# Kernel optimization log

Hardware: AMD Instinct MI355X
Metric: run time of the kernel (lower is better)

## Reference

```python
import jax, jax.numpy as jnp
import numpy as np

NUM_LAYERS = 3

def setup_inputs() -> dict:
    key = jax.random.key(0)
    ks = jax.random.split(key, 9)
    B, T, ND, H, LD, L = 128, 512, 128, 512, 128, NUM_LAYERS
    s = 0.05
    return {
        "noise_seq": jax.random.normal(ks[0], (B, T, ND), jnp.float32),
        "h_coupled": jax.random.normal(ks[1], (L, B, H), jnp.float32),
        "Wx0": jax.random.normal(ks[2], (ND, 4 * H), jnp.float32) * s,
        "Wxr": jax.random.normal(ks[3], (L - 1, H, 4 * H), jnp.float32) * s,
        "Wh": jax.random.normal(ks[4], (L, H, 4 * H), jnp.float32) * s,
        "Wc": jax.random.normal(ks[5], (L, H, 4 * H), jnp.float32) * s,
        "b": jnp.zeros((L, 4 * H), jnp.float32),
        "Wout": jax.random.normal(ks[6], (H, LD), jnp.float32) * s,
        "bout": jnp.zeros((LD,), jnp.float32),
    }

def _cell(x, h, c, h_cpl, Wx, Wh_i, Wc_i, b_i):
    # gates: [B, 4H] = x@Wx + h@Wh + h_cpl@Wc + b
    gates = x @ Wx + h @ Wh_i + h_cpl @ Wc_i + b_i
    i_g, f_g, g_g, o_g = jnp.split(gates, 4, axis=-1)
    c_new = jax.nn.sigmoid(f_g) * c + jax.nn.sigmoid(i_g) * jnp.tanh(g_g)
    h_new = jax.nn.sigmoid(o_g) * jnp.tanh(c_new)
    return h_new, c_new

def reference(noise_seq, h_coupled, Wx0, Wxr, Wh, Wc, b, Wout, bout):
    B, T, _ = noise_seq.shape
    L, _, H = h_coupled.shape

    def step(carry, x_t):
        h, c = carry  # each [L, B, H]
        hs, cs = [], []
        inp = x_t
        for i in range(L):
            Wx = Wx0 if i == 0 else Wxr[i - 1]
            h_new, c_new = _cell(inp, h[i], c[i], h_coupled[i], Wx, Wh[i], Wc[i], b[i])
            hs.append(h_new)
            cs.append(c_new)
            inp = h_new
        out_t = jax.nn.sigmoid(inp @ Wout + bout)  # [B, latent]
        return (jnp.stack(hs), jnp.stack(cs)), out_t

    h0 = jnp.zeros((L, B, H), noise_seq.dtype)
    c0 = jnp.zeros((L, B, H), noise_seq.dtype)
    xs = jnp.swapaxes(noise_seq, 0, 1)  # [T, B, ND]
    (h_fin, _), outs = jax.lax.scan(step, (h0, c0), xs)
    return jnp.swapaxes(outs, 0, 1), h_fin  # [B, T, latent], [L, B, H]
```

## Files before the change

kernel.cpp:

```cpp
#include <hip/hip_runtime.h>
#include <hip/hip_bf16.h>


typedef unsigned short ushort_t;

using frag_ab = __attribute__((ext_vector_type(8))) short;
using frag_cd = __attribute__((ext_vector_type(4))) float;

#define B_   128
#define T_   512
#define ND_  128
#define H_   512
#define G_   2048
#define LD_  128

#define OFF_WHH   0u
#define OFF_WHL   3145728u
#define OFF_WXH   6291456u
#define OFF_WXL   8650752u
#define OFF_WCH   11010048u
#define OFF_WCL   14155776u
#define OFF_WOUT  17301504u
#define OFF_HCH   17367040u
#define OFF_HCL   17563648u
#define OFF_HBH   17760256u
#define OFF_HBL   18153472u
#define OFF_SCR   18546688u
#define USH_BYTES 37224448u
#define FOFF_C     0u
#define FOFF_CTERM 196608u

__device__ inline float sig_(float x)  { return 1.0f / (1.0f + __expf(-x)); }
__device__ inline float tanh_(float x) { return 2.0f / (1.0f + __expf(-2.0f * x)) - 1.0f; }

__device__ inline ushort_t f2b(float f) {
    __hip_bfloat16 h = __float2bfloat16(f);
    return __builtin_bit_cast(unsigned short, h);
}
__device__ inline float b2f(ushort_t u) {
    unsigned int v = ((unsigned int)u) << 16;
    return __builtin_bit_cast(float, v);
}

__global__ void swz_kernel(const float* __restrict__ src,
                           ushort_t* __restrict__ dhi, ushort_t* __restrict__ dlo,
                           int K, int N) {
    int tid = blockIdx.x * 256 + threadIdx.x;
    int total = (K >> 5) * (N >> 4) * 64;
    if (tid >= total) return;
    int lane = tid & 63;
    int rest = tid >> 6;
    int NF = N >> 4;
    int nf = rest % NF;
    int kb = rest / NF;
    int kbase = kb * 32 + (lane >> 4) * 8;
    int n = nf * 16 + (lane & 15);
    union { ushort_t u[8]; uint4 v; } thi, tlo;
#pragma unroll
    for (int j = 0; j < 8; ++j) {
        float v = src[(size_t)(kbase + j) * N + n];
        ushort_t hi = f2b(v);
        thi.u[j] = hi;
        tlo.u[j] = f2b(v - b2f(hi));
    }
    *(uint4*)(dhi + (size_t)tid * 8) = thi.v;
    *(uint4*)(dlo + (size_t)tid * 8) = tlo.v;
}

__global__ void cvt_kernel(const float* __restrict__ src,
                           ushort_t* __restrict__ dhi, ushort_t* __restrict__ dlo, int n) {
    int i = blockIdx.x * 256 + threadIdx.x;
    if (i >= n) return;
    float v = src[i];
    ushort_t hi = f2b(v);
    dhi[i] = hi;
    dlo[i] = f2b(v - b2f(hi));
}

__device__ inline void mfma_seg3(const ushort_t* __restrict__ Ah,
                                 const ushort_t* __restrict__ Al,
                                 const ushort_t* __restrict__ Bh,
                                 const ushort_t* __restrict__ Bl,
                                 int rowA, int cg, int nkb, frag_cd acc[4]) {
    int lane = threadIdx.x & 63;
    int koff = (lane >> 4) * 8;
#pragma unroll 2
    for (int kb = 0; kb < nkb; ++kb) {
        frag_ab ah = *(const frag_ab*)(Ah + (size_t)rowA * H_ + kb * 32 + koff);
        frag_ab al = *(const frag_ab*)(Al + (size_t)rowA * H_ + kb * 32 + koff);
#pragma unroll
        for (int q = 0; q < 4; ++q) {
            size_t bo = ((size_t)(kb * 128 + q * 32 + cg) * 64 + lane) * 8;
            frag_ab bh = *(const frag_ab*)(Bh + bo);
            frag_ab bl = *(const frag_ab*)(Bl + bo);
            acc[q] = __builtin_amdgcn_mfma_f32_16x16x32_bf16(ah, bh, acc[q], 0, 0, 0);
            acc[q] = __builtin_amdgcn_mfma_f32_16x16x32_bf16(ah, bl, acc[q], 0, 0, 0);
            acc[q] = __builtin_amdgcn_mfma_f32_16x16x32_bf16(al, bh, acc[q], 0, 0, 0);
        }
    }
}

__global__ __launch_bounds__(256) void cterm_kernel(char* __restrict__ ws,
                                                    const float* __restrict__ bias) {
    ushort_t* wsU = (ushort_t*)ws;
    float* wsF = (float*)(ws + USH_BYTES);
    int lane = threadIdx.x & 63, w = threadIdx.x >> 6;
    int bid = blockIdx.x;
    int layer = bid >> 6;
    int sub = bid & 63;
    int rg = sub >> 5, cg = sub & 31;
    int m = lane & 15, kq = lane >> 4;
    int r0 = rg * 64 + w * 16;
    int rowA = r0 + m;
    frag_cd acc[4] = {};
    mfma_seg3(wsU + OFF_HCH + layer * 65536, wsU + OFF_HCL + layer * 65536,
              wsU + OFF_WCH + (size_t)layer * 1048576, wsU + OFF_WCL + (size_t)layer * 1048576,
              rowA, cg, 16, acc);
    float* ct = wsF + FOFF_CTERM + (size_t)layer * 262144;
#pragma unroll
    for (int reg = 0; reg < 4; ++reg) {
        int row = r0 + kq * 4 + reg;
#pragma unroll
        for (int q = 0; q < 4; ++q) {
            int gcol = q * 512 + cg * 16 + m;
            ct[(size_t)row * G_ + gcol] = acc[q][reg] + bias[layer * G_ + gcol];
        }
    }
}

__device__ inline void seg_accum64k(const ushort_t* __restrict__ Ah,
                                    const ushort_t* __restrict__ Al,
                                    const ushort_t* __restrict__ Bh,
                                    const ushort_t* __restrict__ Bl,
                                    int r0, int cg, int kb0, int nkb, frag_cd acc[4][4]) {
    int lane = threadIdx.x & 63;
    int m = lane & 15;
    int koff = (lane >> 4) * 8;
#pragma unroll 2
    for (int kb = kb0; kb < kb0 + nkb; ++kb) {
        frag_ab ah[4], al[4];
#pragma unroll
        for (int rt = 0; rt < 4; ++rt) {
            size_t ao = (size_t)(r0 + rt * 16 + m) * H_ + kb * 32 + koff;
            ah[rt] = *(const frag_ab*)(Ah + ao);
            al[rt] = *(const frag_ab*)(Al + ao);
        }
#pragma unroll
        for (int q = 0; q < 4; ++q) {
            size_t bo = ((size_t)(kb * 128 + q * 32 + cg) * 64 + lane) * 8;
            frag_ab bh = *(const frag_ab*)(Bh + bo);
            frag_ab bl = *(const frag_ab*)(Bl + bo);
#pragma unroll
            for (int rt = 0; rt < 4; ++rt) {
                acc[rt][q] = __builtin_amdgcn_mfma_f32_16x16x32_bf16(ah[rt], bh, acc[rt][q], 0, 0, 0);
                acc[rt][q] = __builtin_amdgcn_mfma_f32_16x16x32_bf16(ah[rt], bl, acc[rt][q], 0, 0, 0);
                acc[rt][q] = __builtin_amdgcn_mfma_f32_16x16x32_bf16(al[rt], bh, acc[rt][q], 0, 0, 0);
            }
        }
    }
}

__global__ __launch_bounds__(256) void tick_kernel(const float* __restrict__ noise,
                                                   char* __restrict__ ws,
                                                   float* __restrict__ out,
                                                   const float* __restrict__ bout,
                                                   int tick) {
    __shared__ float ex[4][4096];

    ushort_t* wsU = (ushort_t*)ws;
    float* wsF = (float*)(ws + USH_BYTES);
    int lane = threadIdx.x & 63;
    int w = threadIdx.x >> 6;
    int bid = blockIdx.x;
    int m = lane & 15, kq = lane >> 4;
    int koff = kq * 8;

    if (bid < 192) {
        int rg64 = bid / 96;
        int u = bid % 96;
        int layer = u >> 5;
        int cg = u & 31;
        int s = tick - layer;
        if (s < 0 || s >= T_) return;
        int r0 = rg64 * 64;
        frag_cd acc[4][4] = {};

        if (layer == 0) {
            const ushort_t* Bh = wsU + OFF_WXH;
            const ushort_t* Bl = wsU + OFF_WXL;
            int kb = w;
            frag_ab ah[4], al[4];
#pragma unroll
            for (int rt = 0; rt < 4; ++rt) {
                const float* np = noise +
                    ((size_t)(r0 + rt * 16 + m) * T_ + s) * ND_ + kb * 32 + koff;
                float4 f0 = *(const float4*)np;
                float4 f1 = *(const float4*)(np + 4);
                float xf[8] = {f0.x, f0.y, f0.z, f0.w, f1.x, f1.y, f1.z, f1.w};
#pragma unroll
                for (int j = 0; j < 8; ++j) {
                    ushort_t hi = f2b(xf[j]);
                    ah[rt][j] = (short)hi;
                    al[rt][j] = (short)f2b(xf[j] - b2f(hi));
                }
            }
#pragma unroll
            for (int q = 0; q < 4; ++q) {
                size_t bo = ((size_t)(kb * 128 + q * 32 + cg) * 64 + lane) * 8;
                frag_ab bh = *(const frag_ab*)(Bh + bo);
                frag_ab bl = *(const frag_ab*)(Bl + bo);
#pragma unroll
                for (int rt = 0; rt < 4; ++rt) {
                    acc[rt][q] = __builtin_amdgcn_mfma_f32_16x16x32_bf16(ah[rt], bh, acc[rt][q], 0, 0, 0);
                    acc[rt][q] = __builtin_amdgcn_mfma_f32_16x16x32_bf16(ah[rt], bl, acc[rt][q], 0, 0, 0);
                    acc[rt][q] = __builtin_amdgcn_mfma_f32_16x16x32_bf16(al[rt], bh, acc[rt][q], 0, 0, 0);
                }
            }
        } else {
            unsigned hb = (unsigned)((layer - 1) * 2 + (s & 1)) * 65536u;
            seg_accum64k(wsU + OFF_HBH + hb, wsU + OFF_HBL + hb,
                         wsU + OFF_WXH + 262144u + (size_t)(layer - 1) * 1048576,
                         wsU + OFF_WXL + 262144u + (size_t)(layer - 1) * 1048576,
                         r0, cg, w * 4, 4, acc);
        }
        if (s > 0) {
            unsigned hb = (unsigned)(layer * 2 + ((s - 1) & 1)) * 65536u;
            seg_accum64k(wsU + OFF_HBH + hb, wsU + OFF_HBL + hb,
                         wsU + OFF_WHH + (size_t)layer * 1048576,
                         wsU + OFF_WHL + (size_t)layer * 1048576,
                         r0, cg, w * 4, 4, acc);
        }

        {
            float* eb = &ex[w][0];
#pragma unroll
            for (int rt = 0; rt < 4; ++rt)
#pragma unroll
                for (int q = 0; q < 4; ++q)
#pragma unroll
                    for (int reg = 0; reg < 4; ++reg)
                        eb[(rt * 16 + kq * 4 + reg) * 64 + q * 16 + m] = acc[rt][q][reg];
        }
        __syncthreads();

        const float* ct = wsF + FOFF_CTERM + (size_t)layer * 262144;
        float* cst = wsF + FOFF_C + layer * 65536;
        ushort_t* hhi = wsU + OFF_HBH + (layer * 2 + (s & 1)) * 65536;
        ushort_t* hlo = wsU + OFF_HBL + (layer * 2 + (s & 1)) * 65536;
        int tid = threadIdx.x;
#pragma unroll
        for (int ee = 0; ee < 4; ++ee) {
            int e = tid + ee * 256;
            int row = e >> 4;
            int hcol = e & 15;
            int grow = r0 + row;
            int hc = cg * 16 + hcol;
            int rb = row * 64 + hcol;
            float gi = ex[0][rb +  0] + ex[1][rb +  0] + ex[2][rb +  0] + ex[3][rb +  0];
            float gf = ex[0][rb + 16] + ex[1][rb + 16] + ex[2][rb + 16] + ex[3][rb + 16];
            float gg = ex[0][rb + 32] + ex[1][rb + 32] + ex[2][rb + 32] + ex[3][rb + 32];
            float go = ex[0][rb + 48] + ex[1][rb + 48] + ex[2][rb + 48] + ex[3][rb + 48];
            const float* cr = ct + (size_t)grow * G_ + hc;
            gi += cr[0]; gf += cr[512]; gg += cr[1024]; go += cr[1536];
            float cp = (s > 0) ? cst[grow * H_ + hc] : 0.0f;
            float cn = sig_(gf) * cp + sig_(gi) * tanh_(gg);
            float hn = sig_(go) * tanh_(cn);
            cst[grow * H_ + hc] = cn;
            ushort_t hi = f2b(hn);
            hhi[grow * H_ + hc] = hi;
            hlo[grow * H_ + hc] = f2b(hn - b2f(hi));
            if (s == T_ - 1)
                out[8388608u + (size_t)layer * 65536 + grow * H_ + hc] = hn;
        }
    } else {
        int sp = tick - 3;
        if (sp < 0 || sp >= T_) return;
        int owid = (bid - 192) * 4 + w;
        int rg = owid >> 1;
        int ch = owid & 1;
        int r0o = rg * 32;
        const ushort_t* A  = wsU + OFF_HBH + (4 + (sp & 1)) * 65536;
        const ushort_t* Bw = wsU + OFF_WOUT;
        frag_cd acc[2][4] = {};
#pragma unroll 2
        for (int kb = 0; kb < 16; ++kb) {
            frag_ab a[2];
#pragma unroll
            for (int rt = 0; rt < 2; ++rt)
                a[rt] = *(const frag_ab*)(A + (size_t)(r0o + rt * 16 + m) * H_ + kb * 32 + koff);
#pragma unroll
            for (int cf = 0; cf < 4; ++cf) {
                frag_ab b = *(const frag_ab*)(Bw + ((size_t)(kb * 8 + ch * 4 + cf) * 64 + lane) * 8);
#pragma unroll
                for (int rt = 0; rt < 2; ++rt)
                    acc[rt][cf] = __builtin_amdgcn_mfma_f32_16x16x32_bf16(a[rt], b, acc[rt][cf], 0, 0, 0);
            }
        }
#pragma unroll
        for (int rt = 0; rt < 2; ++rt)
#pragma unroll
            for (int cf = 0; cf < 4; ++cf)
#pragma unroll
                for (int reg = 0; reg < 4; ++reg) {
                    int row = r0o + rt * 16 + kq * 4 + reg;
                    int oc = ch * 64 + cf * 16 + m;
                    out[((size_t)row * T_ + sp) * LD_ + oc] =
                        sig_(acc[rt][cf][reg] + bout[oc]);
                }
    }
}

extern "C" void kernel_launch(void* const* d_in, const int* in_sizes, int n_in,
                              void* d_out, int out_size, void* d_ws, size_t ws_size,
                              hipStream_t stream) {
    const float* noise = (const float*)d_in[0];
    const float* hcpl  = (const float*)d_in[1];
    const float* Wx0   = (const float*)d_in[2];
    const float* Wxr   = (const float*)d_in[3];
    const float* Wh    = (const float*)d_in[4];
    const float* Wc    = (const float*)d_in[5];
    const float* bias  = (const float*)d_in[6];
    const float* Wout  = (const float*)d_in[7];
    const float* bout  = (const float*)d_in[8];
    float* out = (float*)d_out;
    char* ws = (char*)d_ws;
    ushort_t* wsU = (ushort_t*)ws;

    auto launch_swz = [&](const float* src, unsigned ohi, unsigned olo, int K, int N) {
        int total = (K / 32) * (N / 16) * 64;
        swz_kernel<<<(total + 255) / 256, 256, 0, stream>>>(src, wsU + ohi, wsU + olo, K, N);
    };
    for (int l = 0; l < 3; ++l)
        launch_swz(Wh + (size_t)l * H_ * G_, OFF_WHH + l * 1048576u, OFF_WHL + l * 1048576u, H_, G_);
    launch_swz(Wx0, OFF_WXH, OFF_WXL, ND_, G_);
    for (int l = 0; l < 2; ++l)
        launch_swz(Wxr + (size_t)l * H_ * G_, OFF_WXH + 262144u + l * 1048576u,
                   OFF_WXL + 262144u + l * 1048576u, H_, G_);
    for (int l = 0; l < 3; ++l)
        launch_swz(Wc + (size_t)l * H_ * G_, OFF_WCH + l * 1048576u, OFF_WCL + l * 1048576u, H_, G_);
    launch_swz(Wout, OFF_WOUT, OFF_SCR, H_, LD_);
    cvt_kernel<<<(3 * B_ * H_ + 255) / 256, 256, 0, stream>>>(hcpl, wsU + OFF_HCH, wsU + OFF_HCL,
                                                              3 * B_ * H_);
    cterm_kernel<<<192, 256, 0, stream>>>(ws, bias);

    for (int t = 0; t < 515; ++t)
        tick_kernel<<<194, 256, 0, stream>>>(noise, ws, out, bout, t);
}
```

Before: 8.513 ms.

## Replace per-tick launches with persistent kernel using per-step flag dataflow

The 515 per-tick kernel launches are replaced by one persistent kernel of 194 blocks. Each block loops over time steps and waits on per-layer, per-step atomic counters in workspace instead of relying on kernel boundaries. Hidden-state buffers grow from double to quadruple buffering so layers can run up to several steps apart, and the cell state moves from global memory into registers. This removes launch overhead and the global barrier on every tick. In exchange it depends on all 194 blocks being resident at the same time, and adds spin-wait and fence costs.

```diff
diff --git a/kernel.cpp b/kernel.cpp
--- a/kernel.cpp
+++ b/kernel.cpp
@@ -24,11 +24,14 @@
 #define OFF_HCH   17367040u
 #define OFF_HCL   17563648u
 #define OFF_HBH   17760256u
-#define OFF_HBL   18153472u
-#define OFF_SCR   18546688u
-#define USH_BYTES 37224448u
+#define OFF_HBL   18546688u
+#define OFF_SCR   19333120u
+#define USH_BYTES 38797312u
 #define FOFF_C     0u
 #define FOFF_CTERM 196608u
+#define FOFF_FLAGS 983040u
+
+#define FIDX(l2, s) ((((l2) * 512) + (s)) * 16)
 
 __device__ inline float sig_(float x)  { return 1.0f / (1.0f + __expf(-x)); }
 __device__ inline float tanh_(float x) { return 2.0f / (1.0f + __expf(-2.0f * x)) - 1.0f; }
@@ -40,6 +43,11 @@
 __device__ inline float b2f(ushort_t u) {
     unsigned int v = ((unsigned int)u) << 16;
     return __builtin_bit_cast(float, v);
+}
+
+__device__ inline void spin_ge(int* p, int tgt) {
+    while (__hip_atomic_load(p, __ATOMIC_RELAXED, __HIP_MEMORY_SCOPE_AGENT) < tgt)
+        __builtin_amdgcn_s_sleep(1);
 }
 
 __global__ void swz_kernel(const float* __restrict__ src,
@@ -75,6 +83,12 @@
     ushort_t hi = f2b(v);
     dhi[i] = hi;
     dlo[i] = f2b(v - b2f(hi));
+}
+
+__global__ void zero_flags_kernel(char* __restrict__ ws) {
+    int* flg = (int*)(ws + USH_BYTES) + FOFF_FLAGS;
+    int i = blockIdx.x * 256 + threadIdx.x;
+    if (i < 8 * 512 * 16) flg[i] = 0;
 }
 
 __device__ inline void mfma_seg3(const ushort_t* __restrict__ Ah,
@@ -160,15 +174,15 @@
     }
 }
 
-__global__ __launch_bounds__(256) void tick_kernel(const float* __restrict__ noise,
-                                                   char* __restrict__ ws,
-                                                   float* __restrict__ out,
-                                                   const float* __restrict__ bout,
-                                                   int tick) {
+__global__ __launch_bounds__(256) void persist_kernel(const float* __restrict__ noise,
+                                                      char* __restrict__ ws,
+                                                      float* __restrict__ out,
+                                                      const float* __restrict__ bout) {
     __shared__ float ex[4][4096];
 
     ushort_t* wsU = (ushort_t*)ws;
     float* wsF = (float*)(ws + USH_BYTES);
+    int* flg = (int*)wsF + FOFF_FLAGS;
     int lane = threadIdx.x & 63;
     int w = threadIdx.x >> 6;
     int bid = blockIdx.x;
@@ -180,133 +194,160 @@
         int u = bid % 96;
         int layer = u >> 5;
         int cg = u & 31;
-        int s = tick - layer;
-        if (s < 0 || s >= T_) return;
         int r0 = rg64 * 64;
-        frag_cd acc[4][4] = {};
-
-        if (layer == 0) {
-            const ushort_t* Bh = wsU + OFF_WXH;
-            const ushort_t* Bl = wsU + OFF_WXL;
-            int kb = w;
-            frag_ab ah[4], al[4];
-#pragma unroll
-            for (int rt = 0; rt < 4; ++rt) {
-                const float* np = noise +
-                    ((size_t)(r0 + rt * 16 + m) * T_ + s) * ND_ + kb * 32 + koff;
-                float4 f0 = *(const float4*)np;
-                float4 f1 = *(const float4*)(np + 4);
-                float xf[8] = {f0.x, f0.y, f0.z, f0.w, f1.x, f1.y, f1.z, f1.w};
-#pragma unroll
-                for (int j = 0; j < 8; ++j) {
-                    ushort_t hi = f2b(xf[j]);
-                    ah[rt][j] = (short)hi;
-                    al[rt][j] = (short)f2b(xf[j] - b2f(hi));
-                }
-            }
-#pragma unroll
-            for (int q = 0; q < 4; ++q) {
-                size_t bo = ((size_t)(kb * 128 + q * 32 + cg) * 64 + lane) * 8;
-                frag_ab bh = *(const frag_ab*)(Bh + bo);
-                frag_ab bl = *(const frag_ab*)(Bl + bo);
+        int l2 = layer * 2 + rg64;
+        const float* ct = wsF + FOFF_CTERM + (size_t)layer * 262144;
+        float creg[4] = {0.0f, 0.0f, 0.0f, 0.0f};
+
+        for (int s = 0; s < T_; ++s) {
+            if (threadIdx.x == 0) {
+                if (layer > 0) spin_ge(&flg[FIDX(l2 - 2, s)], 32);
+                if (s > 0)     spin_ge(&flg[FIDX(l2, s - 1)], 32);
+                if (s >= 4) {
+                    if (layer < 2) spin_ge(&flg[FIDX(l2 + 2, s - 4)], 32);
+                    else           spin_ge(&flg[FIDX(6 + rg64, s - 4)], 1);
+                }
+                __builtin_amdgcn_fence(__ATOMIC_ACQUIRE, "agent");
+            }
+            __syncthreads();
+
+            frag_cd acc[4][4] = {};
+            if (layer == 0) {
+                const ushort_t* Bh = wsU + OFF_WXH;
+                const ushort_t* Bl = wsU + OFF_WXL;
+                int kb = w;
+                frag_ab ah[4], al[4];
 #pragma unroll
                 for (int rt = 0; rt < 4; ++rt) {
-                    acc[rt][q] = __builtin_amdgcn_mfma_f32_16x16x32_bf16(ah[rt], bh, acc[rt][q], 0, 0, 0);
-                    acc[rt][q] = __builtin_amdgcn_mfma_f32_16x16x32_bf16(ah[rt], bl, acc[rt][q], 0, 0, 0);
-                    acc[rt][q] = __builtin_amdgcn_mfma_f32_16x16x32_bf16(al[rt], bh, acc[rt][q], 0, 0, 0);
-                }
-            }
-        } else {
-            unsigned hb = (unsigned)((layer - 1) * 2 + (s & 1)) * 65536u;
-            seg_accum64k(wsU + OFF_HBH + hb, wsU + OFF_HBL + hb,
-                         wsU + OFF_WXH + 262144u + (size_t)(layer - 1) * 1048576,
-                         wsU + OFF_WXL + 262144u + (size_t)(layer - 1) * 1048576,
-                         r0, cg, w * 4, 4, acc);
-        }
-        if (s > 0) {
-            unsigned hb = (unsigned)(layer * 2 + ((s - 1) & 1)) * 65536u;
-            seg_accum64k(wsU + OFF_HBH + hb, wsU + OFF_HBL + hb,
-                         wsU + OFF_WHH + (size_t)layer * 1048576,
-                         wsU + OFF_WHL + (size_t)layer * 1048576,
-                         r0, cg, w * 4, 4, acc);
-        }
-
-        {
-            float* eb = &ex[w][0];
-#pragma unroll
-            for (int rt = 0; rt < 4; ++rt)
-#pragma unroll
-                for (int q = 0; q < 4; ++q)
-#pragma unroll
-                    for (int reg = 0; reg < 4; ++reg)
-                        eb[(rt * 16 + kq * 4 + reg) * 64 + q * 16 + m] = acc[rt][q][reg];
-        }
-        __syncthreads();
-
-        const float* ct = wsF + FOFF_CTERM + (size_t)layer * 262144;
-        float* cst = wsF + FOFF_C + layer * 65536;
-        ushort_t* hhi = wsU + OFF_HBH + (layer * 2 + (s & 1)) * 65536;
-        ushort_t* hlo = wsU + OFF_HBL + (layer * 2 + (s & 1)) * 65536;
-        int tid = threadIdx.x;
-#pragma unroll
-        for (int ee = 0; ee < 4; ++ee) {
-            int e = tid + ee * 256;
-            int row = e >> 4;
-            int hcol = e & 15;
-            int grow = r0 + row;
-            int hc = cg * 16 + hcol;
-            int rb = row * 64 + hcol;
-            float gi = ex[0][rb +  0] + ex[1][rb +  0] + ex[2][rb +  0] + ex[3][rb +  0];
-            float gf = ex[0][rb + 16] + ex[1][rb + 16] + ex[2][rb + 16] + ex[3][rb + 16];
-            float gg = ex[0][rb + 32] + ex[1][rb + 32] + ex[2][rb + 32] + ex[3][rb + 32];
-            float go = ex[0][rb + 48] + ex[1][rb + 48] + ex[2][rb + 48] + ex[3][rb + 48];
-            const float* cr = ct + (size_t)grow * G_ + hc;
-            gi += cr[0]; gf += cr[512]; gg += cr[1024]; go += cr[1536];
-            float cp = (s > 0) ? cst[grow * H_ + hc] : 0.0f;
-            float cn = sig_(gf) * cp + sig_(gi) * tanh_(gg);
-            float hn = sig_(go) * tanh_(cn);
-            cst[grow * H_ + hc] = cn;
-            ushort_t hi = f2b(hn);
-            hhi[grow * H_ + hc] = hi;
-            hlo[grow * H_ + hc] = f2b(hn - b2f(hi));
-            if (s == T_ - 1)
-                out[8388608u + (size_t)layer * 65536 + grow * H_ + hc] = hn;
+                    const float* np = noise +
+                        ((size_t)(r0 + rt * 16 + m) * T_ + s) * ND_ + kb * 32 + koff;
+                    float4 f0 = *(const float4*)np;
+                    float4 f1 = *(const float4*)(np + 4);
+                    float xf[8] = {f0.x, f0.y, f0.z, f0.w, f1.x, f1.y, f1.z, f1.w};
+#pragma unroll
+                    for (int j = 0; j < 8; ++j) {
+                        ushort_t hi = f2b(xf[j]);
+                        ah[rt][j] = (short)hi;
+                        al[rt][j] = (short)f2b(xf[j] - b2f(hi));
+                    }
+                }
+#pragma unroll
+                for (int q = 0; q < 4; ++q) {
+                    size_t bo = ((size_t)(kb * 128 + q * 32 + cg) * 64 + lane) * 8;
+                    frag_ab bh = *(const frag_ab*)(Bh + bo);
+                    frag_ab bl = *(const frag_ab*)(Bl + bo);
+#pragma unroll
+                    for (int rt = 0; rt < 4; ++rt) {
+                        acc[rt][q] = __builtin_amdgcn_mfma_f32_16x16x32_bf16(ah[rt], bh, acc[rt][q], 0, 0, 0);
+                        acc[rt][q] = __builtin_amdgcn_mfma_f32_16x16x32_bf16(ah[rt], bl, acc[rt][q], 0, 0, 0);
+                        acc[rt][q] = __builtin_amdgcn_mfma_f32_16x16x32_bf16(al[rt], bh, acc[rt][q], 0, 0, 0);
+                    }
+                }
+            } else {
+                unsigned hb = (unsigned)((layer - 1) * 4 + (s & 3)) * 65536u;
+                seg_accum64k(wsU + OFF_HBH + hb, wsU + OFF_HBL + hb,
+                             wsU + OFF_WXH + 262144u + (size_t)(layer - 1) * 1048576,
+                             wsU + OFF_WXL + 262144u + (size_t)(layer - 1) * 1048576,
+                             r0, cg, w * 4, 4, acc);
+            }
+            if (s > 0) {
+                unsigned hb = (unsigned)(layer * 4 + ((s - 1) & 3)) * 65536u;
+                seg_accum64k(wsU + OFF_HBH + hb, wsU + OFF_HBL + hb,
+                             wsU + OFF_WHH + (size_t)layer * 1048576,
+                             wsU + OFF_WHL + (size_t)layer * 1048576,
+                             r0, cg, w * 4, 4, acc);
+            }
+
+            {
+                float* eb = &ex[w][0];
+#pragma unroll
+                for (int rt = 0; rt < 4; ++rt)
+#pragma unroll
+                    for (int q = 0; q < 4; ++q)
+#pragma unroll
+                        for (int reg = 0; reg < 4; ++reg)
+                            eb[(rt * 16 + kq * 4 + reg) * 64 + q * 16 + m] = acc[rt][q][reg];
+            }
+            __syncthreads();
+
+            {
+                ushort_t* hhi = wsU + OFF_HBH + (unsigned)(layer * 4 + (s & 3)) * 65536u;
+                ushort_t* hlo = wsU + OFF_HBL + (unsigned)(layer * 4 + (s & 3)) * 65536u;
+                int tid = threadIdx.x;
+#pragma unroll
+                for (int ee = 0; ee < 4; ++ee) {
+                    int e = tid + ee * 256;
+                    int row = e >> 4;
+                    int hcol = e & 15;
+                    int grow = r0 + row;
+                    int hc = cg * 16 + hcol;
+                    int rb = row * 64 + hcol;
+                    float gi = ex[0][rb +  0] + ex[1][rb +  0] + ex[2][rb +  0] + ex[3][rb +  0];
+                    float gf = ex[0][rb + 16] + ex[1][rb + 16] + ex[2][rb + 16] + ex[3][rb + 16];
+                    float gg = ex[0][rb + 32] + ex[1][rb + 32] + ex[2][rb + 32] + ex[3][rb + 32];
+                    float go = ex[0][rb + 48] + ex[1][rb + 48] + ex[2][rb + 48] + ex[3][rb + 48];
+                    const float* cr = ct + (size_t)grow * G_ + hc;
+                    gi += cr[0]; gf += cr[512]; gg += cr[1024]; go += cr[1536];
+                    float cn = sig_(gf) * creg[ee] + sig_(gi) * tanh_(gg);
+                    float hn = sig_(go) * tanh_(cn);
+                    creg[ee] = cn;
+                    ushort_t hi = f2b(hn);
+                    hhi[grow * H_ + hc] = hi;
+                    hlo[grow * H_ + hc] = f2b(hn - b2f(hi));
+                    if (s == T_ - 1)
+                        out[8388608u + (size_t)layer * 65536 + grow * H_ + hc] = hn;
+                }
+            }
+            __syncthreads();
+            if (threadIdx.x == 0)
+                __hip_atomic_fetch_add(&flg[FIDX(l2, s)], 1,
+                                       __ATOMIC_RELEASE, __HIP_MEMORY_SCOPE_AGENT);
         }
     } else {
-        int sp = tick - 3;
-        if (sp < 0 || sp >= T_) return;
-        int owid = (bid - 192) * 4 + w;
-        int rg = owid >> 1;
-        int ch = owid & 1;
-        int r0o = rg * 32;
-        const ushort_t* A  = wsU + OFF_HBH + (4 + (sp & 1)) * 65536;
-        const ushort_t* Bw = wsU + OFF_WOUT;
-        frag_cd acc[2][4] = {};
+        int g = bid - 192;
+        for (int sp = 0; sp < T_; ++sp) {
+            if (threadIdx.x == 0) {
+                spin_ge(&flg[FIDX(4 + g, sp)], 32);
+                __builtin_amdgcn_fence(__ATOMIC_ACQUIRE, "agent");
+            }
+            __syncthreads();
+            int owid = g * 4 + w;
+            int rg = owid >> 1;
+            int ch = owid & 1;
+            int r0o = rg * 32;
+            const ushort_t* A  = wsU + OFF_HBH + (unsigned)(8 + (sp & 3)) * 65536u;
+            const ushort_t* Bw = wsU + OFF_WOUT;
+            frag_cd acc[2][4] = {};
 #pragma unroll 2
-        for (int kb = 0; kb < 16; ++kb) {
-            frag_ab a[2];
+            for (int kb = 0; kb < 16; ++kb) {
+                frag_ab a[2];
+#pragma unroll
+                for (int rt = 0; rt < 2; ++rt)
+                    a[rt] = *(const frag_ab*)(A + (size_t)(r0o + rt * 16 + m) * H_ + kb * 32 + koff);
+#pragma unroll
+                for (int cf = 0; cf < 4; ++cf) {
+                    frag_ab b = *(const frag_ab*)(Bw + ((size_t)(kb * 8 + ch * 4 + cf) * 64 + lane) * 8);
+#pragma unroll
+                    for (int rt = 0; rt < 2; ++rt)
+                        acc[rt][cf] = __builtin_amdgcn_mfma_f32_16x16x32_bf16(a[rt], b, acc[rt][cf], 0, 0, 0);
+                }
+            }
 #pragma unroll
             for (int rt = 0; rt < 2; ++rt)
-                a[rt] = *(const frag_ab*)(A + (size_t)(r0o + rt * 16 + m) * H_ + kb * 32 + koff);
-#pragma unroll
-            for (int cf = 0; cf < 4; ++cf) {
-                frag_ab b = *(const frag_ab*)(Bw + ((size_t)(kb * 8 + ch * 4 + cf) * 64 + lane) * 8);
-#pragma unroll
-                for (int rt = 0; rt < 2; ++rt)
-                    acc[rt][cf] = __builtin_amdgcn_mfma_f32_16x16x32_bf16(a[rt], b, acc[rt][cf], 0, 0, 0);
-            }
-        }
-#pragma unroll
-        for (int rt = 0; rt < 2; ++rt)
-#pragma unroll
-            for (int cf = 0; cf < 4; ++cf)
-#pragma unroll
-                for (int reg = 0; reg < 4; ++reg) {
-                    int row = r0o + rt * 16 + kq * 4 + reg;
-                    int oc = ch * 64 + cf * 16 + m;
-                    out[((size_t)row * T_ + sp) * LD_ + oc] =
-                        sig_(acc[rt][cf][reg] + bout[oc]);
-                }
+#pragma unroll
+                for (int cf = 0; cf < 4; ++cf)
+#pragma unroll
+                    for (int reg = 0; reg < 4; ++reg) {
+                        int row = r0o + rt * 16 + kq * 4 + reg;
+                        int oc = ch * 64 + cf * 16 + m;
+                        out[((size_t)row * T_ + sp) * LD_ + oc] =
+                            sig_(acc[rt][cf][reg] + bout[oc]);
+                    }
+            __syncthreads();
+            if (threadIdx.x == 0)
+                __hip_atomic_fetch_add(&flg[FIDX(6 + g, sp)], 1,
+                                       __ATOMIC_RELEASE, __HIP_MEMORY_SCOPE_AGENT);
+        }
     }
 }
 
@@ -341,8 +382,8 @@
     launch_swz(Wout, OFF_WOUT, OFF_SCR, H_, LD_);
     cvt_kernel<<<(3 * B_ * H_ + 255) / 256, 256, 0, stream>>>(hcpl, wsU + OFF_HCH, wsU + OFF_HCL,
                                                               3 * B_ * H_);
+    zero_flags_kernel<<<(8 * 512 * 16 + 255) / 256, 256, 0, stream>>>(ws);
     cterm_kernel<<<192, 256, 0, stream>>>(ws, bias);
 
-    for (int t = 0; t < 515; ++t)
-        tick_kernel<<<194, 256, 0, stream>>>(noise, ws, out, bout, t);
-}
+    persist_kernel<<<194, 256, 0, stream>>>(noise, ws, out, bout);
+}
```

Measured after the change: 13.14 ms. 54.4% more time.
